# Performance work log

Measured on AMD Instinct MI355X. Metric: run time of the kernel, lower is better.

Reference implementation:

```python
import jax, jax.numpy as jnp
import numpy as np

HEADS = 16

def setup_inputs() -> dict:
    key = jax.random.key(0)
    ks = jax.random.split(key, 6)
    b, n, d, k = 4, 4096, 1024, 256
    return {
        "x": jax.random.normal(ks[0], (b, n, d), dtype=jnp.float32),
        "Wq": jax.random.normal(ks[1], (d, d), dtype=jnp.float32) * 0.02,
        "Wk": jax.random.normal(ks[2], (d, d), dtype=jnp.float32) * 0.02,
        "Wv": jax.random.normal(ks[3], (d, d), dtype=jnp.float32) * 0.02,
        "proj_k": jax.random.normal(ks[4], (n, k), dtype=jnp.float32) * 0.02,
        "proj_v": jax.random.normal(ks[5], (n, k), dtype=jnp.float32) * 0.02,
    }

def reference(x, Wq, Wk, Wv, proj_k, proj_v):
    b, n, d = x.shape
    h = HEADS
    dh = d // h
    k = proj_k.shape[1]
    # Q/K/V projections (no bias)
    q = jnp.einsum('bnd,de->bne', x, Wq)          # [b,n,d]
    keys = jnp.einsum('bnd,de->bne', x, Wk)       # [b,n,d]
    vals = jnp.einsum('bnd,de->bne', x, Wv)       # [b,n,d]
    # low-rank sequence projection: n -> k
    keys = jnp.einsum('bnd,nk->bkd', keys, proj_k)   # [b,k,d]
    vals = jnp.einsum('bnd,nk->bkd', vals, proj_v)   # [b,k,d]
    # split heads
    q = q.reshape(b, n, h, dh).transpose(0, 2, 1, 3)      # [b,h,n,dh]
    keys = keys.reshape(b, k, h, dh).transpose(0, 2, 1, 3)  # [b,h,k,dh]
    vals = vals.reshape(b, k, h, dh).transpose(0, 2, 1, 3)  # [b,h,k,dh]
    # attention over reduced k dim (NOTE: module applies no 1/sqrt(dh) scale)
    dots = jnp.einsum('bhnd,bhkd->bhnk', q, keys)
    attn = jax.nn.softmax(dots, axis=-1)
    out = jnp.einsum('bhnk,bhkd->bhnd', attn, vals)
    return out.transpose(0, 2, 1, 3).reshape(b, n, d)
```

## Files before the change

kernel.cpp:

```cpp
#include <hip/hip_runtime.h>


typedef __fp16 f16x8 __attribute__((ext_vector_type(8)));
typedef __fp16 f16x2 __attribute__((ext_vector_type(2)));
typedef float fl4 __attribute__((ext_vector_type(4)));
typedef float f32x4 __attribute__((ext_vector_type(4)));
typedef unsigned int u32x2 __attribute__((ext_vector_type(2)));
typedef unsigned int u32x4 __attribute__((ext_vector_type(4)));

#define MFMA16(a, b, c) __builtin_amdgcn_mfma_f32_16x16x32_f16((a), (b), (c), 0, 0, 0)

__device__ __forceinline__ unsigned int pk2u(float a, float b) {
  f16x2 p = __builtin_amdgcn_cvt_pkrtz(a, b);
  return __builtin_bit_cast(unsigned int, p);
}

__device__ __forceinline__ f16x8 pk8(fl4 a, fl4 b) {
  f16x2 p0 = __builtin_amdgcn_cvt_pkrtz(a[0], a[1]);
  f16x2 p1 = __builtin_amdgcn_cvt_pkrtz(a[2], a[3]);
  f16x2 p2 = __builtin_amdgcn_cvt_pkrtz(b[0], b[1]);
  f16x2 p3 = __builtin_amdgcn_cvt_pkrtz(b[2], b[3]);
  f16x8 r;
  r[0] = p0[0]; r[1] = p0[1]; r[2] = p1[0]; r[3] = p1[1];
  r[4] = p2[0]; r[5] = p2[1]; r[6] = p3[0]; r[7] = p3[1];
  return r;
}

__device__ __forceinline__ void gload_lds16(const __fp16* g, void* lds_base) {
  __builtin_amdgcn_global_load_lds(
      (const __attribute__((address_space(1))) void*)g,
      (__attribute__((address_space(3))) void*)lds_base, 16, 0, 0);
}

__device__ __forceinline__ f16x8 rd_swz(const __fp16* base, int row, int lg) {
  return *(const f16x8*)((const char*)base + row * 64 +
                         ((lg ^ ((row >> 1) & 3)) * 16));
}

__device__ __forceinline__ f16x8 rd128(const __fp16* base, int row, int ch) {
  return *(const f16x8*)((const char*)base + row * 128 +
                         ((ch ^ (row & 7)) * 16));
}

__global__ __launch_bounds__(256) void tr_cvt(
    const float* __restrict__ in, __fp16* __restrict__ out, int R, int C) {
  __shared__ float tile[32][33];
  const int t = threadIdx.x;
  const int c0 = blockIdx.x * 32, r0 = blockIdx.y * 32;
  {
    const int r = t >> 3, cg = (t & 7) * 4;
    fl4 v = *(const fl4*)(in + (size_t)(r0 + r) * C + c0 + cg);
    tile[r][cg] = v[0]; tile[r][cg + 1] = v[1];
    tile[r][cg + 2] = v[2]; tile[r][cg + 3] = v[3];
  }
  __syncthreads();
  {
    const int cc = t >> 3, rg = (t & 7) * 4;
    u32x2 p;
    p[0] = pk2u(tile[rg + 0][cc], tile[rg + 1][cc]);
    p[1] = pk2u(tile[rg + 2][cc], tile[rg + 3][cc]);
    *(u32x2*)(out + (size_t)(c0 + cc) * R + r0 + rg) = p;
  }
}

__global__ __launch_bounds__(256) void xprep(
    const float* __restrict__ X, __fp16* __restrict__ Xf,
    __fp16* __restrict__ XT) {
  __shared__ float tile[32][65];
  const int t = threadIdx.x;
  const int n0 = blockIdx.x * 32, d0 = blockIdx.y * 64, b = blockIdx.z;
  const float* src = X + ((size_t)b * 4096 + n0) * 1024 + d0;
  {
    const int r = t >> 3, cg = (t & 7) * 8;
    fl4 v0 = *(const fl4*)(src + (size_t)r * 1024 + cg);
    fl4 v1 = *(const fl4*)(src + (size_t)r * 1024 + cg + 4);
    *(f16x8*)(Xf + ((size_t)b * 4096 + n0 + r) * 1024 + d0 + cg) = pk8(v0, v1);
#pragma unroll
    for (int j = 0; j < 4; ++j) {
      tile[r][cg + j] = v0[j];
      tile[r][cg + 4 + j] = v1[j];
    }
  }
  __syncthreads();
  {
    const int d = t >> 2, ng = (t & 3) * 8;
    fl4 a, c;
#pragma unroll
    for (int j = 0; j < 4; ++j) {
      a[j] = tile[ng + j][d];
      c[j] = tile[ng + 4 + j][d];
    }
    *(f16x8*)(XT + ((size_t)b * 1024 + d0 + d) * 4096 + n0 + ng) = pk8(a, c);
  }
}

__global__ __launch_bounds__(256) void stage1_partial(
    const __fp16* __restrict__ pkT,
    const __fp16* __restrict__ pvT,
    const __fp16* __restrict__ XT,
    float* __restrict__ Pk,
    float* __restrict__ Pv) {
  __shared__ __fp16 Ak[64 * 64];
  __shared__ __fp16 Av[64 * 64];
  __shared__ __fp16 Bx[64 * 64];
  const int t = threadIdx.x;
  const int lane = t & 63, w = t >> 6;
  const int lr = lane & 15, lg = lane >> 4;
  const int fid = blockIdx.x;
  const int g = fid >> 5, s5 = fid & 31;
  const int kk0 = (s5 >> 3) * 64, p8 = s5 & 7;
  const int pr = g * 8 + p8;
  const int dd0 = (pr & 15) * 64;
  const int z = pr >> 4, b = z & 3, c = z >> 2;
  const int wr = (w >> 1) * 32, wc = (w & 1) * 32;

  f32x4 acck[2][2], accv[2][2];
#pragma unroll
  for (int i = 0; i < 2; ++i)
#pragma unroll
    for (int j = 0; j < 2; ++j) {
      acck[i][j] = (f32x4){0.f, 0.f, 0.f, 0.f};
      accv[i][j] = (f32x4){0.f, 0.f, 0.f, 0.f};
    }

  const int r8 = lane >> 3, c8 = lane & 7;
  const int ssw = ((c8 ^ r8) * 8);
  const __fp16* pkS0 = pkT + (size_t)(kk0 + w * 8 + r8) * 4096 + c * 1024 + ssw;
  const __fp16* pkS1 = pkS0 + (size_t)32 * 4096;
  const __fp16* pvS0 = pvT + (size_t)(kk0 + w * 8 + r8) * 4096 + c * 1024 + ssw;
  const __fp16* pvS1 = pvS0 + (size_t)32 * 4096;
  const __fp16* xS0 =
      XT + ((size_t)b * 1024 + dd0 + w * 8 + r8) * 4096 + c * 1024 + ssw;
  const __fp16* xS1 = xS0 + (size_t)32 * 4096;

  for (int it = 0; it < 16; ++it) {
    const int n0 = it * 64;
    __syncthreads();
    gload_lds16(pkS0 + n0, (char*)Ak + w * 1024);
    gload_lds16(pkS1 + n0, (char*)Ak + 4096 + w * 1024);
    gload_lds16(pvS0 + n0, (char*)Av + w * 1024);
    gload_lds16(pvS1 + n0, (char*)Av + 4096 + w * 1024);
    gload_lds16(xS0 + n0, (char*)Bx + w * 1024);
    gload_lds16(xS1 + n0, (char*)Bx + 4096 + w * 1024);
    __syncthreads();

#pragma unroll
    for (int s = 0; s < 2; ++s) {
      f16x8 ak[2], av[2], bx[2];
#pragma unroll
      for (int i = 0; i < 2; ++i) {
        ak[i] = rd128(Ak, wr + i * 16 + lr, s * 4 + lg);
        av[i] = rd128(Av, wr + i * 16 + lr, s * 4 + lg);
      }
#pragma unroll
      for (int j = 0; j < 2; ++j)
        bx[j] = rd128(Bx, wc + j * 16 + lr, s * 4 + lg);
#pragma unroll
      for (int i = 0; i < 2; ++i)
#pragma unroll
        for (int j = 0; j < 2; ++j) {
          acck[i][j] = MFMA16(ak[i], bx[j], acck[i][j]);
          accv[i][j] = MFMA16(av[i], bx[j], accv[i][j]);
        }
    }
  }

#pragma unroll
  for (int i = 0; i < 2; ++i)
#pragma unroll
    for (int j = 0; j < 2; ++j)
#pragma unroll
      for (int r = 0; r < 4; ++r) {
        const size_t row = (size_t)z * 256 + kk0 + wr + i * 16 + lg * 4 + r;
        const int col = dd0 + wc + j * 16 + lr;
        Pk[row * 1024 + col] = acck[i][j][r];
        Pv[row * 1024 + col] = accv[i][j][r];
      }
}

__global__ __launch_bounds__(256) void stage1_reduce(
    const float* __restrict__ Pk, const float* __restrict__ Pv,
    __fp16* __restrict__ Xk, __fp16* __restrict__ Xv) {
  const size_t base = ((size_t)blockIdx.x * 256 + threadIdx.x) * 4;
  const int b = (int)(base >> 18);
  const size_t rem = base & 0x3FFFFu;
  fl4 ak = (fl4){0.f, 0.f, 0.f, 0.f}, av = (fl4){0.f, 0.f, 0.f, 0.f};
#pragma unroll
  for (int c = 0; c < 4; ++c) {
    const size_t off = (((size_t)(c * 4 + b)) << 18) + rem;
    ak += *(const fl4*)(Pk + off);
    av += *(const fl4*)(Pv + off);
  }
  u32x2 pkp, pvp;
  pkp[0] = pk2u(ak[0], ak[1]); pkp[1] = pk2u(ak[2], ak[3]);
  pvp[0] = pk2u(av[0], av[1]); pvp[1] = pk2u(av[2], av[3]);
  *(u32x2*)(Xk + base) = pkp;
  *(u32x2*)(Xv + base) = pvp;
}

__global__ __launch_bounds__(256) void bt64(
    const __fp16* __restrict__ A, long long bsA,
    const __fp16* __restrict__ B, long long bsB,
    __fp16* __restrict__ C, int ldC, long long bsC) {
  constexpr int E = 1024;
  __shared__ __fp16 As[64 * 32];
  __shared__ __fp16 Bs[64 * 32];
  const int t = threadIdx.x;
  const int lane = t & 63, w = t >> 6;
  const int lr = lane & 15, lg = lane >> 4;
  const int i0 = blockIdx.x * 64, j0 = blockIdx.y * 64;
  A += (size_t)blockIdx.z * (size_t)bsA;
  B += (size_t)blockIdx.z * (size_t)bsB;
  C += (size_t)blockIdx.z * (size_t)bsC;
  const int wr = (w >> 1) * 32, wc = (w & 1) * 32;

  f32x4 acc[2][2];
#pragma unroll
  for (int i = 0; i < 2; ++i)
#pragma unroll
    for (int j = 0; j < 2; ++j) acc[i][j] = (f32x4){0.f, 0.f, 0.f, 0.f};

  const int gl_row = w * 16 + (lane >> 2);
  const int gl_ch = (lane & 3) ^ ((lane >> 3) & 3);
  const __fp16* aSrc = A + (size_t)(i0 + gl_row) * E + gl_ch * 8;
  const __fp16* bSrc = B + (size_t)(j0 + gl_row) * E + gl_ch * 8;

  for (int e0 = 0; e0 < E; e0 += 32) {
    __syncthreads();
    gload_lds16(aSrc + e0, (char*)As + w * 1024);
    gload_lds16(bSrc + e0, (char*)Bs + w * 1024);
    __syncthreads();

    f16x8 af[2], bf[2];
#pragma unroll
    for (int i = 0; i < 2; ++i)
      af[i] = rd_swz(As, wr + i * 16 + lr, lg);
#pragma unroll
    for (int j = 0; j < 2; ++j)
      bf[j] = rd_swz(Bs, wc + j * 16 + lr, lg);
#pragma unroll
    for (int i = 0; i < 2; ++i)
#pragma unroll
      for (int j = 0; j < 2; ++j)
        acc[i][j] = MFMA16(af[i], bf[j], acc[i][j]);
  }

#pragma unroll
  for (int i = 0; i < 2; ++i)
#pragma unroll
    for (int j = 0; j < 2; ++j)
#pragma unroll
      for (int r = 0; r < 4; ++r) {
        const int row = i0 + wr + i * 16 + lg * 4 + r;
        const int col = j0 + wc + j * 16 + lr;
        C[(size_t)row * ldC + col] = (__fp16)acc[i][j][r];
      }
}

__global__ __launch_bounds__(256) void gemm_q(
    const __fp16* __restrict__ Xf,
    const __fp16* __restrict__ WT,
    __fp16* __restrict__ Q) {
  constexpr int K = 1024, N = 1024;
  __shared__ __fp16 Xs[128 * 64];
  __shared__ __fp16 Ws[128 * 64];
  const int t = threadIdx.x;
  const int lane = t & 63, w = t >> 6;
  const int lr = lane & 15, lg = lane >> 4;
  const int fid = blockIdx.x;
  const int g = fid >> 6, s6 = fid & 63;
  const int n0 = (s6 >> 3) * 128;
  const int m0 = (g * 8 + (s6 & 7)) * 128;
  const int wr = (w >> 1) * 64, wc = (w & 1) * 64;

  f32x4 acc[4][4];
#pragma unroll
  for (int i = 0; i < 4; ++i)
#pragma unroll
    for (int j = 0; j < 4; ++j) acc[i][j] = (f32x4){0.f, 0.f, 0.f, 0.f};

  const int r8 = lane >> 3, c8 = lane & 7;
  const int ssw = ((c8 ^ r8) * 8);
  const __fp16* xS = Xf + (size_t)(m0 + w * 8 + r8) * K + ssw;
  const __fp16* wS = WT + (size_t)(n0 + w * 8 + r8) * K + ssw;

  for (int it = 0; it < 16; ++it) {
    const int k0 = it * 64;
    __syncthreads();
#pragma unroll
    for (int i = 0; i < 4; ++i) {
      gload_lds16(xS + (size_t)i * 32 * K + k0, (char*)Xs + i * 4096 + w * 1024);
      gload_lds16(wS + (size_t)i * 32 * K + k0, (char*)Ws + i * 4096 + w * 1024);
    }
    __syncthreads();

#pragma unroll
    for (int s = 0; s < 2; ++s) {
      f16x8 af[4], bf[4];
#pragma unroll
      for (int i = 0; i < 4; ++i)
        af[i] = rd128(Xs, wr + i * 16 + lr, s * 4 + lg);
#pragma unroll
      for (int j = 0; j < 4; ++j)
        bf[j] = rd128(Ws, wc + j * 16 + lr, s * 4 + lg);
#pragma unroll
      for (int i = 0; i < 4; ++i)
#pragma unroll
        for (int j = 0; j < 4; ++j)
          acc[i][j] = MFMA16(af[i], bf[j], acc[i][j]);
    }
  }

#pragma unroll
  for (int i = 0; i < 4; ++i)
#pragma unroll
    for (int j = 0; j < 4; ++j)
#pragma unroll
      for (int r = 0; r < 4; ++r) {
        const int row = m0 + wr + i * 16 + lg * 4 + r;
        const int col = n0 + wc + j * 16 + lr;
        Q[(size_t)row * N + col] = (__fp16)acc[i][j][r];
      }
}

__global__ __launch_bounds__(256) void attn_k(
    const __fp16* __restrict__ Q,
    const __fp16* __restrict__ Kp,
    const __fp16* __restrict__ Vpt,
    float* __restrict__ O) {
  __shared__ __fp16 KV[256 * 64];
  const int t = threadIdx.x;
  const int lane = t & 63, w = t >> 6;
  const int lr = lane & 15, lg = lane >> 4;
  const int bh = blockIdx.x >> 5, rb = blockIdx.x & 31;
  const int b = bh >> 4, h = bh & 15;
  const int m0 = rb * 128 + w * 32;

  const __fp16* Kph = Kp + (size_t)b * 256 * 1024 + h * 64;
  const __fp16* Vph = Vpt + ((size_t)b * 1024 + h * 64) * 256;
  const __fp16* Qh = Q + ((size_t)(b * 4096 + m0)) * 1024 + h * 64;

#pragma unroll
  for (int i = 0; i < 8; ++i) {
    const int kr = (i * 4 + w) * 8 + (lane >> 3);
    gload_lds16(Kph + (size_t)kr * 1024 + (((lane & 7) ^ (kr & 7)) * 8),
                (char*)KV + (i * 4 + w) * 1024);
  }

  f16x8 aq[2][2];
#pragma unroll
  for (int mi = 0; mi < 2; ++mi)
#pragma unroll
    for (int s = 0; s < 2; ++s)
      aq[mi][s] =
          *(const f16x8*)(Qh + (size_t)(mi * 16 + lr) * 1024 + s * 32 + lg * 8);

  __syncthreads();

  f32x4 dots[2][16];
#pragma unroll
  for (int mi = 0; mi < 2; ++mi)
#pragma unroll
    for (int jt = 0; jt < 16; ++jt) dots[mi][jt] = (f32x4){0.f, 0.f, 0.f, 0.f};
#pragma unroll
  for (int jt = 0; jt < 16; ++jt) {
    const int r = jt * 16 + lr;
    f16x8 k0 = *(const f16x8*)((const char*)KV + r * 128 + ((lg ^ (r & 7)) * 16));
    f16x8 k1 =
        *(const f16x8*)((const char*)KV + r * 128 + (((4 + lg) ^ (r & 7)) * 16));
    dots[0][jt] = MFMA16(k0, aq[0][0], dots[0][jt]);
    dots[0][jt] = MFMA16(k1, aq[0][1], dots[0][jt]);
    dots[1][jt] = MFMA16(k0, aq[1][0], dots[1][jt]);
    dots[1][jt] = MFMA16(k1, aq[1][1], dots[1][jt]);
  }

  unsigned cpk[2][16][2];
  float smv[2];
#pragma unroll
  for (int mi = 0; mi < 2; ++mi) {
    float mx = -1e30f;
#pragma unroll
    for (int jt = 0; jt < 16; ++jt)
#pragma unroll
      for (int r = 0; r < 4; ++r) mx = fmaxf(mx, dots[mi][jt][r]);
    mx = fmaxf(mx, __shfl_xor(mx, 16, 64));
    mx = fmaxf(mx, __shfl_xor(mx, 32, 64));
    float sm = 0.f;
#pragma unroll
    for (int jt = 0; jt < 16; ++jt) {
#pragma unroll
      for (int r = 0; r < 4; ++r) {
        float p = __expf(dots[mi][jt][r] - mx);
        dots[mi][jt][r] = p;
        sm += p;
      }
      cpk[mi][jt][0] = pk2u(dots[mi][jt][0], dots[mi][jt][1]);
      cpk[mi][jt][1] = pk2u(dots[mi][jt][2], dots[mi][jt][3]);
    }
    sm += __shfl_xor(sm, 16, 64);
    sm += __shfl_xor(sm, 32, 64);
    smv[mi] = sm;
  }

  __syncthreads();

#pragma unroll
  for (int i = 0; i < 8; ++i) {
    const int dd = (i * 4 + w) * 2 + (lane >> 5);
    gload_lds16(Vph + (size_t)dd * 256 + (((lane & 31) ^ (dd & 7)) * 8),
                (char*)KV + (i * 4 + w) * 1024);
  }
  __syncthreads();

#pragma unroll
  for (int mi = 0; mi < 2; ++mi) {
    f32x4 o[4];
#pragma unroll
    for (int j = 0; j < 4; ++j) o[j] = (f32x4){0.f, 0.f, 0.f, 0.f};
#pragma unroll
    for (int ks = 0; ks < 8; ++ks) {
      u32x4 wds;
#pragma unroll
      for (int m = 0; m < 4; ++m) {
        const int addr = ((((lane & 16) >> 3) + (m >> 1)) * 16 + lr) * 4;
        const int a0 = __builtin_amdgcn_ds_bpermute(
            addr, (int)cpk[mi][ks * 2][m & 1]);
        const int a1 = __builtin_amdgcn_ds_bpermute(
            addr, (int)cpk[mi][ks * 2 + 1][m & 1]);
        wds[m] = (unsigned)((lg >> 1) ? a1 : a0);
      }
      f16x8 pa = __builtin_bit_cast(f16x8, wds);
#pragma unroll
      for (int jt2 = 0; jt2 < 4; ++jt2) {
        const int dd = jt2 * 16 + lr;
        f16x8 bv = *(const f16x8*)((const char*)KV + dd * 512 +
                                   (((ks * 4 + lg) ^ (dd & 7)) * 16));
        o[jt2] = MFMA16(pa, bv, o[jt2]);
      }
    }

    float rs[4];
#pragma unroll
    for (int r = 0; r < 4; ++r)
      rs[r] = 1.f / __shfl(smv[mi], (lane & 48) + lg * 4 + r, 64);
#pragma unroll
    for (int jt2 = 0; jt2 < 4; ++jt2)
#pragma unroll
      for (int r = 0; r < 4; ++r) {
        const size_t row = (size_t)(b * 4096 + m0 + mi * 16 + lg * 4 + r);
        O[row * 1024 + h * 64 + jt2 * 16 + lr] = o[jt2][r] * rs[r];
      }
  }
}

extern "C" void kernel_launch(void* const* d_in, const int* in_sizes, int n_in,
                              void* d_out, int out_size, void* d_ws, size_t ws_size,
                              hipStream_t stream) {
  (void)in_sizes; (void)n_in; (void)out_size; (void)ws_size;
  const float* x  = (const float*)d_in[0];
  const float* Wq = (const float*)d_in[1];
  const float* Wk = (const float*)d_in[2];
  const float* Wv = (const float*)d_in[3];
  const float* pk = (const float*)d_in[4];
  const float* pv = (const float*)d_in[5];
  float* out = (float*)d_out;

  __fp16* Qh  = (__fp16*)d_ws;
  __fp16* WqT = Qh  + (size_t)16384 * 1024;
  __fp16* WkT = WqT + (size_t)1024 * 1024;
  __fp16* WvT = WkT + (size_t)1024 * 1024;
  __fp16* pkT = WvT + (size_t)1024 * 1024;
  __fp16* pvT = pkT + (size_t)256 * 4096;
  __fp16* Xk  = pvT + (size_t)256 * 4096;
  __fp16* Xv  = Xk  + (size_t)4 * 256 * 1024;
  __fp16* Kp  = Xv  + (size_t)4 * 256 * 1024;
  __fp16* Vpt = Kp  + (size_t)4 * 256 * 1024;
  float* Pk = (float*)d_ws;
  float* Pv = Pk + (size_t)16 * 256 * 1024;
  __fp16* Xf16 = (__fp16*)d_out;
  __fp16* XT   = Xf16 + (size_t)4 * 4096 * 1024;

  const dim3 bb(256);

  xprep<<<dim3(128, 16, 4), bb, 0, stream>>>(x, Xf16, XT);
  tr_cvt<<<dim3(32, 32), bb, 0, stream>>>(Wq, WqT, 1024, 1024);
  tr_cvt<<<dim3(32, 32), bb, 0, stream>>>(Wk, WkT, 1024, 1024);
  tr_cvt<<<dim3(32, 32), bb, 0, stream>>>(Wv, WvT, 1024, 1024);
  tr_cvt<<<dim3(8, 128), bb, 0, stream>>>(pk, pkT, 4096, 256);
  tr_cvt<<<dim3(8, 128), bb, 0, stream>>>(pv, pvT, 4096, 256);

  stage1_partial<<<dim3(1024), bb, 0, stream>>>(pkT, pvT, XT, Pk, Pv);
  stage1_reduce<<<dim3(1024), bb, 0, stream>>>(Pk, Pv, Xk, Xv);

  bt64<<<dim3(4, 16, 4), bb, 0, stream>>>(Xk, 256LL * 1024, WkT, 0LL,
                                          Kp, 1024, 256LL * 1024);
  bt64<<<dim3(16, 4, 4), bb, 0, stream>>>(WvT, 0LL, Xv, 256LL * 1024,
                                          Vpt, 256, 1024LL * 256);

  gemm_q<<<dim3(1024), bb, 0, stream>>>(Xf16, WqT, Qh);

  attn_k<<<dim3(2048), bb, 0, stream>>>(Qh, Kp, Vpt, out);
}
```

Measured before the change: 189.2 us.

## Merge prep kernels, fp16 split-K partials, fuse K/V projection GEMMs with wider K-tile

The X conversion/transpose and five weight/projection transposes now run in one launch that dispatches on block index. The split-K partials of the sequence projection are stored as fp16 instead of fp32, which halves partial-sum traffic and lets the reduce kernel process 8 elements per thread. The two small K and V projection GEMMs become one launch with a 64-wide K-tile and 128-byte swizzled LDS reads, halving the barrier count. Storing partials in fp16 adds rounding and overflow risk before the reduction.

```diff
diff --git a/kernel.cpp b/kernel.cpp
--- a/kernel.cpp
+++ b/kernel.cpp
@@ -32,65 +32,78 @@
       (__attribute__((address_space(3))) void*)lds_base, 16, 0, 0);
 }
 
-__device__ __forceinline__ f16x8 rd_swz(const __fp16* base, int row, int lg) {
-  return *(const f16x8*)((const char*)base + row * 64 +
-                         ((lg ^ ((row >> 1) & 3)) * 16));
-}
-
 __device__ __forceinline__ f16x8 rd128(const __fp16* base, int row, int ch) {
   return *(const f16x8*)((const char*)base + row * 128 +
                          ((ch ^ (row & 7)) * 16));
 }
 
-__global__ __launch_bounds__(256) void tr_cvt(
-    const float* __restrict__ in, __fp16* __restrict__ out, int R, int C) {
-  __shared__ float tile[32][33];
+__device__ __forceinline__ void tr_cvt_body(
+    float* tile, const float* in, __fp16* out, int R, int C, int bx, int by) {
   const int t = threadIdx.x;
-  const int c0 = blockIdx.x * 32, r0 = blockIdx.y * 32;
+  const int c0 = bx * 32, r0 = by * 32;
   {
     const int r = t >> 3, cg = (t & 7) * 4;
     fl4 v = *(const fl4*)(in + (size_t)(r0 + r) * C + c0 + cg);
-    tile[r][cg] = v[0]; tile[r][cg + 1] = v[1];
-    tile[r][cg + 2] = v[2]; tile[r][cg + 3] = v[3];
+    tile[r * 33 + cg] = v[0]; tile[r * 33 + cg + 1] = v[1];
+    tile[r * 33 + cg + 2] = v[2]; tile[r * 33 + cg + 3] = v[3];
   }
   __syncthreads();
   {
     const int cc = t >> 3, rg = (t & 7) * 4;
     u32x2 p;
-    p[0] = pk2u(tile[rg + 0][cc], tile[rg + 1][cc]);
-    p[1] = pk2u(tile[rg + 2][cc], tile[rg + 3][cc]);
+    p[0] = pk2u(tile[(rg + 0) * 33 + cc], tile[(rg + 1) * 33 + cc]);
+    p[1] = pk2u(tile[(rg + 2) * 33 + cc], tile[(rg + 3) * 33 + cc]);
     *(u32x2*)(out + (size_t)(c0 + cc) * R + r0 + rg) = p;
   }
 }
 
-__global__ __launch_bounds__(256) void xprep(
+__global__ __launch_bounds__(256) void prep(
     const float* __restrict__ X, __fp16* __restrict__ Xf,
-    __fp16* __restrict__ XT) {
-  __shared__ float tile[32][65];
+    __fp16* __restrict__ XT,
+    const float* __restrict__ Wq, const float* __restrict__ Wk,
+    const float* __restrict__ Wv, __fp16* __restrict__ WqT,
+    __fp16* __restrict__ WkT, __fp16* __restrict__ WvT,
+    const float* __restrict__ pk, const float* __restrict__ pv,
+    __fp16* __restrict__ pkT, __fp16* __restrict__ pvT) {
+  __shared__ float tile[32 * 65];
+  const int id = blockIdx.x;
   const int t = threadIdx.x;
-  const int n0 = blockIdx.x * 32, d0 = blockIdx.y * 64, b = blockIdx.z;
-  const float* src = X + ((size_t)b * 4096 + n0) * 1024 + d0;
-  {
-    const int r = t >> 3, cg = (t & 7) * 8;
-    fl4 v0 = *(const fl4*)(src + (size_t)r * 1024 + cg);
-    fl4 v1 = *(const fl4*)(src + (size_t)r * 1024 + cg + 4);
-    *(f16x8*)(Xf + ((size_t)b * 4096 + n0 + r) * 1024 + d0 + cg) = pk8(v0, v1);
-#pragma unroll
-    for (int j = 0; j < 4; ++j) {
-      tile[r][cg + j] = v0[j];
-      tile[r][cg + 4 + j] = v1[j];
-    }
-  }
-  __syncthreads();
-  {
-    const int d = t >> 2, ng = (t & 3) * 8;
-    fl4 a, c;
-#pragma unroll
-    for (int j = 0; j < 4; ++j) {
-      a[j] = tile[ng + j][d];
-      c[j] = tile[ng + 4 + j][d];
-    }
-    *(f16x8*)(XT + ((size_t)b * 1024 + d0 + d) * 4096 + n0 + ng) = pk8(a, c);
+  if (id < 8192) {
+    const int n0 = (id & 127) * 32, d0 = ((id >> 7) & 15) * 64, b = id >> 11;
+    const float* src = X + ((size_t)b * 4096 + n0) * 1024 + d0;
+    {
+      const int r = t >> 3, cg = (t & 7) * 8;
+      fl4 v0 = *(const fl4*)(src + (size_t)r * 1024 + cg);
+      fl4 v1 = *(const fl4*)(src + (size_t)r * 1024 + cg + 4);
+      *(f16x8*)(Xf + ((size_t)b * 4096 + n0 + r) * 1024 + d0 + cg) = pk8(v0, v1);
+#pragma unroll
+      for (int j = 0; j < 4; ++j) {
+        tile[r * 65 + cg + j] = v0[j];
+        tile[r * 65 + cg + 4 + j] = v1[j];
+      }
+    }
+    __syncthreads();
+    {
+      const int d = t >> 2, ng = (t & 3) * 8;
+      fl4 a, c;
+#pragma unroll
+      for (int j = 0; j < 4; ++j) {
+        a[j] = tile[(ng + j) * 65 + d];
+        c[j] = tile[(ng + 4 + j) * 65 + d];
+      }
+      *(f16x8*)(XT + ((size_t)b * 1024 + d0 + d) * 4096 + n0 + ng) = pk8(a, c);
+    }
+  } else if (id < 11264) {
+    const int idx = id - 8192;
+    const int z = idx >> 10;
+    const float* in = (z == 0) ? Wq : (z == 1) ? Wk : Wv;
+    __fp16* out = (z == 0) ? WqT : (z == 1) ? WkT : WvT;
+    tr_cvt_body(tile, in, out, 1024, 1024, idx & 31, (idx >> 5) & 31);
+  } else {
+    const int idx = id - 11264;
+    const int z = idx >> 10;
+    tr_cvt_body(tile, z ? pv : pk, z ? pvT : pkT, 4096, 256, idx & 7,
+                (idx >> 3) & 127);
   }
 }
 
@@ -98,8 +111,8 @@
     const __fp16* __restrict__ pkT,
     const __fp16* __restrict__ pvT,
     const __fp16* __restrict__ XT,
-    float* __restrict__ Pk,
-    float* __restrict__ Pv) {
+    __fp16* __restrict__ Pk,
+    __fp16* __restrict__ Pv) {
   __shared__ __fp16 Ak[64 * 64];
   __shared__ __fp16 Av[64 * 64];
   __shared__ __fp16 Bx[64 * 64];
@@ -173,45 +186,67 @@
       for (int r = 0; r < 4; ++r) {
         const size_t row = (size_t)z * 256 + kk0 + wr + i * 16 + lg * 4 + r;
         const int col = dd0 + wc + j * 16 + lr;
-        Pk[row * 1024 + col] = acck[i][j][r];
-        Pv[row * 1024 + col] = accv[i][j][r];
+        Pk[row * 1024 + col] = (__fp16)acck[i][j][r];
+        Pv[row * 1024 + col] = (__fp16)accv[i][j][r];
       }
 }
 
 __global__ __launch_bounds__(256) void stage1_reduce(
-    const float* __restrict__ Pk, const float* __restrict__ Pv,
+    const __fp16* __restrict__ Pk, const __fp16* __restrict__ Pv,
     __fp16* __restrict__ Xk, __fp16* __restrict__ Xv) {
-  const size_t base = ((size_t)blockIdx.x * 256 + threadIdx.x) * 4;
-  const int b = (int)(base >> 18);
-  const size_t rem = base & 0x3FFFFu;
-  fl4 ak = (fl4){0.f, 0.f, 0.f, 0.f}, av = (fl4){0.f, 0.f, 0.f, 0.f};
+  const size_t idx = ((size_t)blockIdx.x * 256 + threadIdx.x) * 8;
+  const int b = (int)(idx >> 18);
+  const size_t rem = idx & 0x3FFFFu;
+  float sk[8], sv[8];
+#pragma unroll
+  for (int j = 0; j < 8; ++j) { sk[j] = 0.f; sv[j] = 0.f; }
 #pragma unroll
   for (int c = 0; c < 4; ++c) {
     const size_t off = (((size_t)(c * 4 + b)) << 18) + rem;
-    ak += *(const fl4*)(Pk + off);
-    av += *(const fl4*)(Pv + off);
-  }
-  u32x2 pkp, pvp;
-  pkp[0] = pk2u(ak[0], ak[1]); pkp[1] = pk2u(ak[2], ak[3]);
-  pvp[0] = pk2u(av[0], av[1]); pvp[1] = pk2u(av[2], av[3]);
-  *(u32x2*)(Xk + base) = pkp;
-  *(u32x2*)(Xv + base) = pvp;
-}
-
-__global__ __launch_bounds__(256) void bt64(
-    const __fp16* __restrict__ A, long long bsA,
-    const __fp16* __restrict__ B, long long bsB,
-    __fp16* __restrict__ C, int ldC, long long bsC) {
+    f16x8 vk = *(const f16x8*)(Pk + off);
+    f16x8 vv = *(const f16x8*)(Pv + off);
+#pragma unroll
+    for (int j = 0; j < 8; ++j) {
+      sk[j] += (float)vk[j];
+      sv[j] += (float)vv[j];
+    }
+  }
+  f16x8 ok, ov;
+#pragma unroll
+  for (int j = 0; j < 8; ++j) {
+    ok[j] = (__fp16)sk[j];
+    ov[j] = (__fp16)sv[j];
+  }
+  *(f16x8*)(Xk + idx) = ok;
+  *(f16x8*)(Xv + idx) = ov;
+}
+
+__global__ __launch_bounds__(256) void bt64z(
+    const __fp16* __restrict__ Xk, const __fp16* __restrict__ WkT,
+    __fp16* __restrict__ Kp, const __fp16* __restrict__ WvT,
+    const __fp16* __restrict__ Xv, __fp16* __restrict__ Vpt) {
   constexpr int E = 1024;
-  __shared__ __fp16 As[64 * 32];
-  __shared__ __fp16 Bs[64 * 32];
+  __shared__ __fp16 As[64 * 64];
+  __shared__ __fp16 Bs[64 * 64];
   const int t = threadIdx.x;
   const int lane = t & 63, w = t >> 6;
   const int lr = lane & 15, lg = lane >> 4;
-  const int i0 = blockIdx.x * 64, j0 = blockIdx.y * 64;
-  A += (size_t)blockIdx.z * (size_t)bsA;
-  B += (size_t)blockIdx.z * (size_t)bsB;
-  C += (size_t)blockIdx.z * (size_t)bsC;
+  int id = blockIdx.x;
+  const __fp16 *A, *B;
+  __fp16* C;
+  int i0, j0, ldC;
+  if (id < 256) {
+    const int x = id & 3, y = (id >> 2) & 15, z = id >> 6;
+    A = Xk + (size_t)z * 256 * 1024; B = WkT;
+    C = Kp + (size_t)z * 256 * 1024;
+    i0 = x * 64; j0 = y * 64; ldC = 1024;
+  } else {
+    id -= 256;
+    const int x = id & 15, y = (id >> 4) & 3, z = id >> 6;
+    A = WvT; B = Xv + (size_t)z * 256 * 1024;
+    C = Vpt + (size_t)z * 1024 * 256;
+    i0 = x * 64; j0 = y * 64; ldC = 256;
+  }
   const int wr = (w >> 1) * 32, wc = (w & 1) * 32;
 
   f32x4 acc[2][2];
@@ -220,29 +255,37 @@
 #pragma unroll
     for (int j = 0; j < 2; ++j) acc[i][j] = (f32x4){0.f, 0.f, 0.f, 0.f};
 
-  const int gl_row = w * 16 + (lane >> 2);
-  const int gl_ch = (lane & 3) ^ ((lane >> 3) & 3);
-  const __fp16* aSrc = A + (size_t)(i0 + gl_row) * E + gl_ch * 8;
-  const __fp16* bSrc = B + (size_t)(j0 + gl_row) * E + gl_ch * 8;
-
-  for (int e0 = 0; e0 < E; e0 += 32) {
-    __syncthreads();
-    gload_lds16(aSrc + e0, (char*)As + w * 1024);
-    gload_lds16(bSrc + e0, (char*)Bs + w * 1024);
-    __syncthreads();
-
-    f16x8 af[2], bf[2];
-#pragma unroll
-    for (int i = 0; i < 2; ++i)
-      af[i] = rd_swz(As, wr + i * 16 + lr, lg);
-#pragma unroll
-    for (int j = 0; j < 2; ++j)
-      bf[j] = rd_swz(Bs, wc + j * 16 + lr, lg);
-#pragma unroll
-    for (int i = 0; i < 2; ++i)
+  const int r8 = lane >> 3, c8 = lane & 7;
+  const int ssw = ((c8 ^ r8) * 8);
+  const __fp16* aS0 = A + (size_t)(i0 + w * 8 + r8) * E + ssw;
+  const __fp16* aS1 = aS0 + (size_t)32 * E;
+  const __fp16* bS0 = B + (size_t)(j0 + w * 8 + r8) * E + ssw;
+  const __fp16* bS1 = bS0 + (size_t)32 * E;
+
+  for (int it = 0; it < 16; ++it) {
+    const int e0 = it * 64;
+    __syncthreads();
+    gload_lds16(aS0 + e0, (char*)As + w * 1024);
+    gload_lds16(aS1 + e0, (char*)As + 4096 + w * 1024);
+    gload_lds16(bS0 + e0, (char*)Bs + w * 1024);
+    gload_lds16(bS1 + e0, (char*)Bs + 4096 + w * 1024);
+    __syncthreads();
+
+#pragma unroll
+    for (int s = 0; s < 2; ++s) {
+      f16x8 af[2], bf[2];
+#pragma unroll
+      for (int i = 0; i < 2; ++i)
+        af[i] = rd128(As, wr + i * 16 + lr, s * 4 + lg);
 #pragma unroll
       for (int j = 0; j < 2; ++j)
-        acc[i][j] = MFMA16(af[i], bf[j], acc[i][j]);
+        bf[j] = rd128(Bs, wc + j * 16 + lr, s * 4 + lg);
+#pragma unroll
+      for (int i = 0; i < 2; ++i)
+#pragma unroll
+        for (int j = 0; j < 2; ++j)
+          acc[i][j] = MFMA16(af[i], bf[j], acc[i][j]);
+    }
   }
 
 #pragma unroll
@@ -475,27 +518,20 @@
   __fp16* Xv  = Xk  + (size_t)4 * 256 * 1024;
   __fp16* Kp  = Xv  + (size_t)4 * 256 * 1024;
   __fp16* Vpt = Kp  + (size_t)4 * 256 * 1024;
-  float* Pk = (float*)d_ws;
-  float* Pv = Pk + (size_t)16 * 256 * 1024;
+  __fp16* Pk16 = (__fp16*)d_ws;
+  __fp16* Pv16 = Pk16 + (size_t)16 * 256 * 1024;
   __fp16* Xf16 = (__fp16*)d_out;
   __fp16* XT   = Xf16 + (size_t)4 * 4096 * 1024;
 
   const dim3 bb(256);
 
-  xprep<<<dim3(128, 16, 4), bb, 0, stream>>>(x, Xf16, XT);
-  tr_cvt<<<dim3(32, 32), bb, 0, stream>>>(Wq, WqT, 1024, 1024);
-  tr_cvt<<<dim3(32, 32), bb, 0, stream>>>(Wk, WkT, 1024, 1024);
-  tr_cvt<<<dim3(32, 32), bb, 0, stream>>>(Wv, WvT, 1024, 1024);
-  tr_cvt<<<dim3(8, 128), bb, 0, stream>>>(pk, pkT, 4096, 256);
-  tr_cvt<<<dim3(8, 128), bb, 0, stream>>>(pv, pvT, 4096, 256);
-
-  stage1_partial<<<dim3(1024), bb, 0, stream>>>(pkT, pvT, XT, Pk, Pv);
-  stage1_reduce<<<dim3(1024), bb, 0, stream>>>(Pk, Pv, Xk, Xv);
-
-  bt64<<<dim3(4, 16, 4), bb, 0, stream>>>(Xk, 256LL * 1024, WkT, 0LL,
-                                          Kp, 1024, 256LL * 1024);
-  bt64<<<dim3(16, 4, 4), bb, 0, stream>>>(WvT, 0LL, Xv, 256LL * 1024,
-                                          Vpt, 256, 1024LL * 256);
+  prep<<<dim3(13312), bb, 0, stream>>>(x, Xf16, XT, Wq, Wk, Wv, WqT, WkT, WvT,
+                                       pk, pv, pkT, pvT);
+
+  stage1_partial<<<dim3(1024), bb, 0, stream>>>(pkT, pvT, XT, Pk16, Pv16);
+  stage1_reduce<<<dim3(512), bb, 0, stream>>>(Pk16, Pv16, Xk, Xv);
+
+  bt64z<<<dim3(512), bb, 0, stream>>>(Xk, WkT, Kp, WvT, Xv, Vpt);
 
   gemm_q<<<dim3(1024), bb, 0, stream>>>(Xf16, WqT, Qh);
 
```

New measurement: 166.7 us. 1.14x faster.
